# Optimization experiments

Measured on AMD Instinct MI355X. Metric: run time of the kernel, lower is better.

The kernel has to match this reference:

```python
import jax, jax.numpy as jnp
import numpy as np

NUM_NODES = 100000
NUM_EDGES = 1600000
NUM_GRAPHS = 64
NUM_FEATURES = 128
DIM = 128
OUTPUT_SIZE = 16


def setup_inputs() -> dict:
    key = jax.random.key(0)
    ks = jax.random.split(key, 7)
    features = jax.random.normal(ks[0], (NUM_NODES, NUM_FEATURES), dtype=jnp.float32)
    W1 = jax.random.normal(ks[1], (NUM_FEATURES, DIM), dtype=jnp.float32) / np.sqrt(NUM_FEATURES)
    W2 = jax.random.normal(ks[2], (DIM, DIM), dtype=jnp.float32) / np.sqrt(DIM)
    W3 = jax.random.normal(ks[3], (DIM, OUTPUT_SIZE), dtype=jnp.float32) / np.sqrt(DIM)
    src = jax.random.randint(ks[4], (NUM_EDGES,), 0, NUM_NODES, dtype=jnp.int32)
    dst = jax.random.randint(ks[5], (NUM_EDGES,), 0, NUM_NODES, dtype=jnp.int32)
    graph_ids = jnp.sort(jax.random.randint(ks[6], (NUM_NODES,), 0, NUM_GRAPHS, dtype=jnp.int32))
    return {"features": features, "W1": W1, "W2": W2, "W3": W3,
            "src": src, "dst": dst, "graph_ids": graph_ids}


def _graph_conv(x, W, src, dst, num_nodes):
    # DGL GraphConv, norm='none', bias=False: h_v = sum_{u -> v} (x_u @ W)
    xw = x @ W                      # [N, dim]
    msg = xw[src]                   # gather per edge [E, dim]
    return jax.ops.segment_sum(msg, dst, num_segments=num_nodes)


def reference(features, W1, W2, W3, src, dst, graph_ids):
    n = features.shape[0]
    h = jax.nn.relu(_graph_conv(features, W1, src, dst, n))  # conv1 + ReLU
    h = _graph_conv(h, W2, src, dst, n)                      # conv2
    # dgl.mean_nodes: per-graph mean over nodes
    sums = jax.ops.segment_sum(h, graph_ids, num_segments=NUM_GRAPHS)          # [G, dim]
    counts = jax.ops.segment_sum(jnp.ones((n,), h.dtype), graph_ids,
                                 num_segments=NUM_GRAPHS)                       # [G]
    pooled = sums / jnp.maximum(counts, 1.0)[:, None]
    out = pooled @ W3                                         # fc1 (no bias)
    return jax.nn.sigmoid(out)                                # torch.sigmoid activation
```

## Files before the change

### kernel.cpp

```cpp
#include <hip/hip_runtime.h>

#define FNX 4
#define CSLOT 32
#define OVCAP 65536
#define AP_CHUNK 128

typedef short bf16x8 __attribute__((ext_vector_type(8)));
typedef float f32x4  __attribute__((ext_vector_type(4)));

union U4S8 { uint4 u; bf16x8 s; };

__device__ __forceinline__ unsigned int f2bf(float f) {
    unsigned int u = __float_as_uint(f);
    return (u + 0x7fffu + ((u >> 16) & 1u)) >> 16;
}
__device__ __forceinline__ float bflo(unsigned int u) { return __uint_as_float(u << 16); }
__device__ __forceinline__ float bfhi(unsigned int u) { return __uint_as_float(u & 0xffff0000u); }

__device__ __forceinline__ f32x4 nt_ld_f4(const float4* p) {
    return __builtin_nontemporal_load((const f32x4*)p);
}

__global__ __launch_bounds__(256) void fconv(
    const float4* __restrict__ F4, uint4* __restrict__ B4, long long n8)
{
    long long t = (long long)blockIdx.x * 256 + threadIdx.x;
    if (t >= n8) return;
    f32x4 a = nt_ld_f4(&F4[2 * t]);
    f32x4 b = nt_ld_f4(&F4[2 * t + 1]);
    uint4 o;
    o.x = f2bf(a.x) | (f2bf(a.y) << 16);
    o.y = f2bf(a.z) | (f2bf(a.w) << 16);
    o.z = f2bf(b.x) | (f2bf(b.y) << 16);
    o.w = f2bf(b.z) | (f2bf(b.w) << 16);
    B4[t] = o;
}

__global__ __launch_bounds__(256) void fillfix_xcd(
    const int* __restrict__ src, const int* __restrict__ dst,
    int* __restrict__ cnt, int* __restrict__ col,
    int* __restrict__ ovd, int* __restrict__ ovs, int* __restrict__ ov_cnt,
    int E, int N)
{
    int x  = blockIdx.x & (FNX - 1);
    int bi = blockIdx.x >> 2;
    int K  = gridDim.x >> 2;
    int chunk = (N + FNX - 1) / FNX;
    int lo = x * chunk;
    int hi = lo + chunk; if (hi > N) hi = N;
    for (int e = bi * 256 + threadIdx.x; e < E; e += K * 256) {
        int d = dst[e];
        if (d >= lo && d < hi) {
            int s = src[e];
            int pos = atomicAdd(&cnt[d], 1);
            if (pos < CSLOT) {
                col[(size_t)d * CSLOT + pos] = s;
            } else {
                int op = atomicAdd(ov_cnt, 1);
                if (op < OVCAP) { ovd[op] = d; ovs[op] = s; }
            }
        }
    }
}

__global__ __launch_bounds__(256) void csr_agg_bf16(
    const uint4* __restrict__ X, const int* __restrict__ cnt,
    const int* __restrict__ col,
    const int* __restrict__ ovd, const int* __restrict__ ovs,
    const int* __restrict__ ov_cnt,
    uint4* __restrict__ T, int N)
{
    int v = blockIdx.x * 16 + (threadIdx.x >> 4);
    if (v >= N) return;
    int lane = threadIdx.x & 15;
    int c = cnt[v];
    int end = c < CSLOT ? c : CSLOT;
    const int* cb = col + (size_t)v * CSLOT;
    float a0=0,a1=0,a2=0,a3=0,a4=0,a5=0,a6=0,a7=0;
    #define ACCUM(u) { \
        a0 += bflo((u).x); a1 += bfhi((u).x); \
        a2 += bflo((u).y); a3 += bfhi((u).y); \
        a4 += bflo((u).z); a5 += bfhi((u).z); \
        a6 += bflo((u).w); a7 += bfhi((u).w); }
    int i = 0;
    for (; i + 1 < end; i += 2) {
        int c0 = cb[i], c1 = cb[i + 1];
        uint4 x0 = X[(size_t)c0 * 16 + lane];
        uint4 x1 = X[(size_t)c1 * 16 + lane];
        ACCUM(x0) ACCUM(x1)
    }
    if (i < end) {
        uint4 x0 = X[(size_t)cb[i] * 16 + lane];
        ACCUM(x0)
    }
    int oc = *ov_cnt; if (oc > OVCAP) oc = OVCAP;
    for (int k = 0; k < oc; ++k) {
        if (ovd[k] == v) {
            uint4 x0 = X[(size_t)ovs[k] * 16 + lane];
            ACCUM(x0)
        }
    }
    #undef ACCUM
    uint4 o;
    o.x = f2bf(a0) | (f2bf(a1) << 16);
    o.y = f2bf(a2) | (f2bf(a3) << 16);
    o.z = f2bf(a4) | (f2bf(a5) << 16);
    o.w = f2bf(a6) | (f2bf(a7) << 16);
    T[(size_t)v * 16 + lane] = o;
}

__global__ __launch_bounds__(256) void gemm_mfma(
    const uint4* __restrict__ T, const float* __restrict__ W,
    uint4* __restrict__ Y2q, int N, int RB)
{
    __shared__ char sWT[32768];
    __shared__ unsigned short sT[4][16 * 128];
    int t = threadIdx.x;
    {
        int c = t & 127;
        int xo = (c & 7) << 4;
        #pragma unroll
        for (int i = 0; i < 8; ++i) {
            int kc = (t >> 7) + 2 * i;
            int k0 = kc * 8;
            unsigned int h[8];
            #pragma unroll
            for (int j = 0; j < 8; ++j)
                h[j] = f2bf(W[(k0 + j) * 128 + c]);
            uint4 pk;
            pk.x = h[0] | (h[1] << 16);
            pk.y = h[2] | (h[3] << 16);
            pk.z = h[4] | (h[5] << 16);
            pk.w = h[6] | (h[7] << 16);
            *(uint4*)(sWT + c * 256 + ((k0 * 2) ^ xo)) = pk;
        }
    }
    __syncthreads();

    int wid = t >> 6, l = t & 63;
    int rb = blockIdx.x * 4 + wid;
    if (rb >= RB) return;
    int lrow = l & 15, lg = l >> 4;
    int row = rb * 16 + lrow;

    U4S8 cv;
    bf16x8 a[4];
    #pragma unroll
    for (int kk = 0; kk < 4; ++kk) {
        cv.u = (row < N) ? T[(size_t)row * 16 + kk * 4 + lg] : make_uint4(0,0,0,0);
        a[kk] = cv.s;
    }

    f32x4 acc[8];
    #pragma unroll
    for (int ct = 0; ct < 8; ++ct) acc[ct] = (f32x4){0.f,0.f,0.f,0.f};

    #pragma unroll
    for (int ct = 0; ct < 8; ++ct) {
        int c = ct * 16 + lrow;
        const char* base = sWT + c * 256;
        int xo = (c & 7) << 4;
        #pragma unroll
        for (int kk = 0; kk < 4; ++kk) {
            cv.u = *(const uint4*)(base + ((kk * 64 + lg * 16) ^ xo));
            acc[ct] = __builtin_amdgcn_mfma_f32_16x16x32_bf16(a[kk], cv.s, acc[ct], 0, 0, 0);
        }
    }

    unsigned short* st = sT[wid];
    #pragma unroll
    for (int ct = 0; ct < 8; ++ct) {
        #pragma unroll
        for (int r4 = 0; r4 < 4; ++r4)
            st[(lg * 4 + r4) * 128 + ct * 16 + lrow] =
                (unsigned short)f2bf(fmaxf(acc[ct][r4], 0.f));
    }
    #pragma unroll
    for (int r = 0; r < 4; ++r) {
        int rr = r * 4 + lg;
        uint4 q = *(const uint4*)(st + rr * 128 + lrow * 8);
        Y2q[((size_t)rb * 16 + rr) * 16 + lrow] = q;
    }
}

__global__ __launch_bounds__(512) void agg2pool(
    const uint4* __restrict__ Y2q, const int* __restrict__ cnt,
    const int* __restrict__ col,
    const int* __restrict__ ovd, const int* __restrict__ ovs,
    const int* __restrict__ ov_cnt, const int* __restrict__ gid,
    float* __restrict__ pooled, int N)
{
    __shared__ float sp[64 * 128];
    int t = threadIdx.x;
    #pragma unroll
    for (int i = t; i < 8192; i += 512) sp[i] = 0.f;
    __syncthreads();

    int v0 = blockIdx.x * AP_CHUNK;
    int v1 = v0 + AP_CHUNK; if (v1 > N) v1 = N;
    if (v0 >= N) return;
    int lane = t & 15;
    int oc = *ov_cnt; if (oc > OVCAP) oc = OVCAP;

    for (int v = v0 + (t >> 4); v < v1; v += 32) {
        int c = cnt[v];
        int end = c < CSLOT ? c : CSLOT;
        const int* cb = col + (size_t)v * CSLOT;
        float a0=0,a1=0,a2=0,a3=0,a4=0,a5=0,a6=0,a7=0;
        #define ACCUM(u) { \
            a0 += bflo((u).x); a1 += bfhi((u).x); \
            a2 += bflo((u).y); a3 += bfhi((u).y); \
            a4 += bflo((u).z); a5 += bfhi((u).z); \
            a6 += bflo((u).w); a7 += bfhi((u).w); }
        int i = 0;
        for (; i + 1 < end; i += 2) {
            int s0 = cb[i], s1 = cb[i + 1];
            uint4 y0 = Y2q[(size_t)s0 * 16 + lane];
            uint4 y1 = Y2q[(size_t)s1 * 16 + lane];
            ACCUM(y0) ACCUM(y1)
        }
        if (i < end) {
            uint4 y0 = Y2q[(size_t)cb[i] * 16 + lane];
            ACCUM(y0)
        }
        for (int k = 0; k < oc; ++k) {
            if (ovd[k] == v) {
                uint4 y0 = Y2q[(size_t)ovs[k] * 16 + lane];
                ACCUM(y0)
            }
        }
        #undef ACCUM
        float* b = &sp[gid[v] * 128 + lane * 8];
        atomicAdd(&b[0], a0); atomicAdd(&b[1], a1);
        atomicAdd(&b[2], a2); atomicAdd(&b[3], a3);
        atomicAdd(&b[4], a4); atomicAdd(&b[5], a5);
        atomicAdd(&b[6], a6); atomicAdd(&b[7], a7);
    }
    __syncthreads();

    int gLo = gid[v0];
    int gHi = gid[v1 - 1];
    int nb = (gHi - gLo + 1) * 128;
    int base = gLo * 128;
    for (int i = t; i < nb; i += 512)
        unsafeAtomicAdd(&pooled[base + i], sp[base + i]);
}

__global__ __launch_bounds__(1024) void final_fused(
    const float* __restrict__ pooled, const int* __restrict__ gid, int N,
    const float* __restrict__ W2, const float* __restrict__ W3,
    float* __restrict__ out)
{
    __shared__ float sW23[128 * 16];
    __shared__ int lb[65];
    int t = threadIdx.x;
    if (t <= 64) {
        int lo = 0, hi = N;
        while (lo < hi) { int mid = (lo + hi) >> 1; if (gid[mid] < t) lo = mid + 1; else hi = mid; }
        lb[t] = lo;
    }
    for (int idx = t; idx < 2048; idx += 1024) {
        int k = idx >> 4, o = idx & 15;
        float a = 0.f;
        #pragma unroll 16
        for (int jj = 0; jj < 128; ++jj)
            a += W2[k * 128 + jj] * W3[jj * 16 + o];
        sW23[idx] = a;
    }
    __syncthreads();
    int g = t >> 4, o = t & 15;
    float cntf = fmaxf((float)(lb[g + 1] - lb[g]), 1.0f);
    float acc = 0.f;
    #pragma unroll 16
    for (int k = 0; k < 128; ++k)
        acc += pooled[g * 128 + k] * sW23[k * 16 + o];
    acc /= cntf;
    out[g * 16 + o] = 1.0f / (1.0f + __expf(-acc));
}

extern "C" void kernel_launch(void* const* d_in, const int* in_sizes, int n_in,
                              void* d_out, int out_size, void* d_ws, size_t ws_size,
                              hipStream_t stream)
{
    const float* features = (const float*)d_in[0];
    const float* W1       = (const float*)d_in[1];
    const float* W2       = (const float*)d_in[2];
    const float* W3       = (const float*)d_in[3];
    const int*   src      = (const int*)d_in[4];
    const int*   dst      = (const int*)d_in[5];
    const int*   gid      = (const int*)d_in[6];
    int N = in_sizes[0] / 128;
    int E = in_sizes[4];
    float* out = (float*)d_out;

    int RB = (N + 15) / 16;

    char* ws = (char*)d_ws;
    size_t p = 0;
    auto alloc = [&](size_t bytes) { void* r = ws + p; p = (p + bytes + 255) & ~(size_t)255; return r; };
    unsigned int* fbf  = (unsigned int*)alloc((size_t)N * 128 * 2);
    unsigned int* tbf  = (unsigned int*)alloc((size_t)N * 128 * 2);
    uint4*        Y2q  = (uint4*)alloc((size_t)RB * 16 * 128 * 2);
    int*   col    = (int*)alloc((size_t)N * CSLOT * sizeof(int));
    int*   ovd    = (int*)alloc((size_t)OVCAP * sizeof(int));
    int*   ovs    = (int*)alloc((size_t)OVCAP * sizeof(int));
    size_t cntB = (((size_t)N * 4) + 255) & ~(size_t)255;
    char*  zr   = (char*)alloc(cntB + 256 + 64 * 128 * 4);
    int*   cnt    = (int*)zr;
    int*   ov_cnt = (int*)(zr + cntB);
    float* pooled = (float*)(zr + cntB + 256);

    int aggGrid  = (N + 15) / 16;
    int fillGrid = 2048;
    int gGrid    = (RB + 3) / 4;
    int apGrid   = (N + AP_CHUNK - 1) / AP_CHUNK;
    long long n8 = (long long)N * 16;

    fconv<<<(int)((n8 + 255) / 256), 256, 0, stream>>>((const float4*)features, (uint4*)fbf, n8);

    (void)hipMemsetAsync(zr, 0, cntB + 256 + 64 * 128 * 4, stream);
    fillfix_xcd<<<fillGrid, 256, 0, stream>>>(src, dst, cnt, col, ovd, ovs, ov_cnt, E, N);

    csr_agg_bf16<<<aggGrid, 256, 0, stream>>>((const uint4*)fbf, cnt, col, ovd, ovs, ov_cnt, (uint4*)tbf, N);
    gemm_mfma<<<gGrid, 256, 0, stream>>>((const uint4*)tbf, W1, Y2q, N, RB);

    agg2pool<<<apGrid, 512, 0, stream>>>(Y2q, cnt, col, ovd, ovs, ov_cnt, gid, pooled, N);

    final_fused<<<1, 1024, 0, stream>>>(pooled, gid, N, W2, W3, out);
}
```

Measured before the change: 320.0 us.

## Shrink pooling LDS bins, halve chunk size, and unroll gathers by four

The pooling aggregation kernel now keeps only 8 graph bins in shared memory, offset from the chunk's first graph id, instead of all 64. This cuts LDS use so more blocks can be resident, and it falls back to global atomics when a chunk spans more graphs than that. The chunk size is halved so more blocks launch, and both gather loops now read four column indices with one int4 load and issue four row loads per iteration for more memory-level parallelism. The early return for out-of-range blocks was removed, which assumes the grid is sized exactly to N.

```diff
diff --git a/kernel.cpp b/kernel.cpp
--- a/kernel.cpp
+++ b/kernel.cpp
@@ -3,7 +3,8 @@
 #define FNX 4
 #define CSLOT 32
 #define OVCAP 65536
-#define AP_CHUNK 128
+#define AP_CHUNK 64
+#define AP_GBINS 8
 
 typedef short bf16x8 __attribute__((ext_vector_type(8)));
 typedef float f32x4  __attribute__((ext_vector_type(4)));
@@ -83,13 +84,15 @@
         a4 += bflo((u).z); a5 += bfhi((u).z); \
         a6 += bflo((u).w); a7 += bfhi((u).w); }
     int i = 0;
-    for (; i + 1 < end; i += 2) {
-        int c0 = cb[i], c1 = cb[i + 1];
-        uint4 x0 = X[(size_t)c0 * 16 + lane];
-        uint4 x1 = X[(size_t)c1 * 16 + lane];
-        ACCUM(x0) ACCUM(x1)
-    }
-    if (i < end) {
+    for (; i + 3 < end; i += 4) {
+        int4 cc = *(const int4*)(cb + i);
+        uint4 x0 = X[(size_t)cc.x * 16 + lane];
+        uint4 x1 = X[(size_t)cc.y * 16 + lane];
+        uint4 x2 = X[(size_t)cc.z * 16 + lane];
+        uint4 x3 = X[(size_t)cc.w * 16 + lane];
+        ACCUM(x0) ACCUM(x1) ACCUM(x2) ACCUM(x3)
+    }
+    for (; i < end; ++i) {
         uint4 x0 = X[(size_t)cb[i] * 16 + lane];
         ACCUM(x0)
     }
@@ -190,15 +193,17 @@
     const int* __restrict__ ov_cnt, const int* __restrict__ gid,
     float* __restrict__ pooled, int N)
 {
-    __shared__ float sp[64 * 128];
+    __shared__ float sp[AP_GBINS * 128];
     int t = threadIdx.x;
-    #pragma unroll
-    for (int i = t; i < 8192; i += 512) sp[i] = 0.f;
-    __syncthreads();
-
     int v0 = blockIdx.x * AP_CHUNK;
     int v1 = v0 + AP_CHUNK; if (v1 > N) v1 = N;
-    if (v0 >= N) return;
+    int gLo = gid[v0];
+    int gHi = gid[v1 - 1];
+    bool fits = (gHi - gLo) < AP_GBINS;
+    #pragma unroll
+    for (int i = t; i < AP_GBINS * 128; i += 512) sp[i] = 0.f;
+    __syncthreads();
+
     int lane = t & 15;
     int oc = *ov_cnt; if (oc > OVCAP) oc = OVCAP;
 
@@ -213,13 +218,15 @@
             a4 += bflo((u).z); a5 += bfhi((u).z); \
             a6 += bflo((u).w); a7 += bfhi((u).w); }
         int i = 0;
-        for (; i + 1 < end; i += 2) {
-            int s0 = cb[i], s1 = cb[i + 1];
-            uint4 y0 = Y2q[(size_t)s0 * 16 + lane];
-            uint4 y1 = Y2q[(size_t)s1 * 16 + lane];
-            ACCUM(y0) ACCUM(y1)
-        }
-        if (i < end) {
+        for (; i + 3 < end; i += 4) {
+            int4 cc = *(const int4*)(cb + i);
+            uint4 y0 = Y2q[(size_t)cc.x * 16 + lane];
+            uint4 y1 = Y2q[(size_t)cc.y * 16 + lane];
+            uint4 y2 = Y2q[(size_t)cc.z * 16 + lane];
+            uint4 y3 = Y2q[(size_t)cc.w * 16 + lane];
+            ACCUM(y0) ACCUM(y1) ACCUM(y2) ACCUM(y3)
+        }
+        for (; i < end; ++i) {
             uint4 y0 = Y2q[(size_t)cb[i] * 16 + lane];
             ACCUM(y0)
         }
@@ -230,20 +237,27 @@
             }
         }
         #undef ACCUM
-        float* b = &sp[gid[v] * 128 + lane * 8];
-        atomicAdd(&b[0], a0); atomicAdd(&b[1], a1);
-        atomicAdd(&b[2], a2); atomicAdd(&b[3], a3);
-        atomicAdd(&b[4], a4); atomicAdd(&b[5], a5);
-        atomicAdd(&b[6], a6); atomicAdd(&b[7], a7);
+        if (fits) {
+            float* b = &sp[(gid[v] - gLo) * 128 + lane * 8];
+            atomicAdd(&b[0], a0); atomicAdd(&b[1], a1);
+            atomicAdd(&b[2], a2); atomicAdd(&b[3], a3);
+            atomicAdd(&b[4], a4); atomicAdd(&b[5], a5);
+            atomicAdd(&b[6], a6); atomicAdd(&b[7], a7);
+        } else {
+            float* b = &pooled[gid[v] * 128 + lane * 8];
+            unsafeAtomicAdd(&b[0], a0); unsafeAtomicAdd(&b[1], a1);
+            unsafeAtomicAdd(&b[2], a2); unsafeAtomicAdd(&b[3], a3);
+            unsafeAtomicAdd(&b[4], a4); unsafeAtomicAdd(&b[5], a5);
+            unsafeAtomicAdd(&b[6], a6); unsafeAtomicAdd(&b[7], a7);
+        }
     }
     __syncthreads();
 
-    int gLo = gid[v0];
-    int gHi = gid[v1 - 1];
-    int nb = (gHi - gLo + 1) * 128;
-    int base = gLo * 128;
-    for (int i = t; i < nb; i += 512)
-        unsafeAtomicAdd(&pooled[base + i], sp[base + i]);
+    if (fits) {
+        int nb = (gHi - gLo + 1) * 128;
+        for (int i = t; i < nb; i += 512)
+            unsafeAtomicAdd(&pooled[gLo * 128 + i], sp[i]);
+    }
 }
 
 __global__ __launch_bounds__(1024) void final_fused(
```

New measurement: 302.2 us. -5.6%, faster.
